# Kernel tuning notes

Measured on AMD Instinct MI355X. Metric: run time of the kernel, lower is better.

Reference implementation:

```python
import jax, jax.numpy as jnp
import numpy as np

N_LBL, E_LBL, K = 32, 16, 16          # node labels, edge labels, tensor_neurons
DN, DE = 2 * N_LBL, 2 * E_LBL         # TNM input dims
REG = [16, 8, 4]                      # reg_neurons
N = M = 6000


def setup_inputs() -> dict:
    key = jax.random.key(0)
    ks = jax.random.split(key, 24)
    u = lambda k, s: jax.random.uniform(k, s, dtype=jnp.float32)
    g = lambda k, s: jax.random.normal(k, s, dtype=jnp.float32) * 0.1
    inp = dict(
        emb1=u(ks[0], (N, N_LBL)), emb2=u(ks[1], (N, N_LBL)),
        adj1=u(ks[2], (N, N)), adj2=u(ks[3], (N, N)),
        edge_attr1=u(ks[4], (M, E_LBL)), edge_attr2=u(ks[5], (M, E_LBL)),
        edge_adj1=u(ks[6], (M, M)), edge_adj2=u(ks[7], (M, M)),
        avg_v=jnp.float32(50.0),
        # tensor networks: nc, in, ie share D=DN (stacked on axis 0); ec uses DE
        Wn=g(ks[8], (3, DN, DN, K)), Wbn=g(ks[9], (3, K, 2 * DN)), bn=g(ks[10], (3, K)),
        We=g(ks[11], (DE, DE, K)), Wbe=g(ks[12], (K, 2 * DE)), be=g(ks[13], (K,)),
        # 4 MLP stacks (order nc, in, ie, ec), torch Linear layout [out, in]
        mlp1_w=g(ks[14], (4, REG[0], K)), mlp1_b=g(ks[15], (4, REG[0])),
        mlp2_w=g(ks[16], (4, REG[1], REG[0])), mlp2_b=g(ks[17], (4, REG[1])),
        mlp3_w=g(ks[18], (4, REG[2], REG[1])), mlp3_b=g(ks[19], (4, REG[2])),
        score_w=g(ks[20], (4, REG[2])), score_b=g(ks[21], (4,)),
    )
    return inp


def _tnm(e1, e2, W, Wb, b):
    # SimGNN-style bilinear tensor network on pooled vectors e1,e2: [D]
    scoring = jnp.einsum('d,dek,e->k', e1, W, e2)
    block = Wb @ jnp.concatenate([e1, e2])
    return jax.nn.relu(scoring + block + b)  # [K]


def reference(emb1, emb2, adj1, adj2, edge_attr1, edge_attr2, edge_adj1, edge_adj2,
              avg_v, Wn, Wbn, bn, We, Wbe, be,
              mlp1_w, mlp1_b, mlp2_w, mlp2_b, mlp3_w, mlp3_b, score_w, score_b):
    def gal_pass(adj, feat):
        h1 = adj @ feat          # GraphAggregationLayer: mm(adj, input)
        h2 = adj @ h1
        return h1, h2

    g1h1, g1h2 = gal_pass(adj1, emb1)
    g2h1, g2h2 = gal_pass(adj2, emb2)
    e1h1, _ = gal_pass(edge_adj1, edge_attr1)
    e2h1, _ = gal_pass(edge_adj2, edge_attr2)

    # concat + sum-pool -> single vectors of width 2D
    g1_01 = jnp.concatenate([emb1, g1h1], axis=1).sum(0)   # [DN]
    g2_01 = jnp.concatenate([emb2, g2h1], axis=1).sum(0)
    g1_12 = jnp.concatenate([g1h1, g1h2], axis=1).sum(0)
    g2_12 = jnp.concatenate([g2h1, g2h2], axis=1).sum(0)
    e1_01 = jnp.concatenate([edge_attr1, e1h1], axis=1).sum(0)  # [DE]
    e2_01 = jnp.concatenate([edge_attr2, e2h1], axis=1).sum(0)

    # node branches nc, in (use 01 pooled) and ie (uses 12 pooled)
    e1s = jnp.stack([g1_01, g1_01, g1_12])
    e2s = jnp.stack([g2_01, g2_01, g2_12])
    s_node = jax.vmap(_tnm)(e1s, e2s, Wn, Wbn, bn)          # [3, K]
    s_ec = _tnm(e1_01, e2_01, We, Wbe, be)                  # [K]
    s = jnp.concatenate([s_node, s_ec[None]], axis=0)       # [4, K] (nc,in,ie,ec)

    h = jax.nn.relu(jnp.einsum('boi,bi->bo', mlp1_w, s) + mlp1_b)
    h = jax.nn.relu(jnp.einsum('boi,bi->bo', mlp2_w, h) + mlp2_b)
    h = jax.nn.relu(jnp.einsum('boi,bi->bo', mlp3_w, h) + mlp3_b)
    scores4 = jax.nn.sigmoid(jnp.einsum('bi,bi->b', score_w, h) + score_b)  # [4]

    # final order: nc, in, ec, ie
    score = scores4[jnp.array([0, 1, 3, 2])]
    pre_ged = jnp.sum(-jnp.log(score) * avg_v)              # target_mode == 'exp'
    pre_sim = jnp.exp(-pre_ged / avg_v)
    return pre_sim, pre_ged, score
```

## Files before the change

### kernel.cpp

```cpp
#include <hip/hip_runtime.h>
#include <cstdint>
#include <cmath>

#define THREADS 256
#define LDP 6016
#define RGROUPS 8
#define SLAB_R 32

template <bool WEIGHTED>
__global__ __launch_bounds__(THREADS, 8)
void colsum_tile_kernel(const float* __restrict__ A0,
                        const float* __restrict__ A1,
                        const float* __restrict__ w0,
                        const float* __restrict__ w1,
                        float* __restrict__ P,
                        int N, int nSlabs, int R) {
    const int z = blockIdx.z;
    const float* __restrict__ A = z ? A1 : A0;
    const float* __restrict__ wv = z ? w1 : w0;

    const int col = blockIdx.x * (THREADS * 4) + threadIdx.x * 4;
    if (col >= N) return;
    const int slab = blockIdx.y;
    int r0 = slab * R;
    int r1 = r0 + R;
    if (r1 > N) r1 = N;

    float ax = 0.f, ay = 0.f, az = 0.f, aw = 0.f;
    float bx = 0.f, by = 0.f, bz = 0.f, bw = 0.f;
    const float* p = A + (size_t)r0 * N + col;
    const size_t sN = (size_t)N;
    int r = r0;
    for (; r + 8 <= r1; r += 8, p += 8 * sN) {
        float4 v0 = *reinterpret_cast<const float4*>(p + 0 * sN);
        float4 v1 = *reinterpret_cast<const float4*>(p + 1 * sN);
        float4 v2 = *reinterpret_cast<const float4*>(p + 2 * sN);
        float4 v3 = *reinterpret_cast<const float4*>(p + 3 * sN);
        float4 v4 = *reinterpret_cast<const float4*>(p + 4 * sN);
        float4 v5 = *reinterpret_cast<const float4*>(p + 5 * sN);
        float4 v6 = *reinterpret_cast<const float4*>(p + 6 * sN);
        float4 v7 = *reinterpret_cast<const float4*>(p + 7 * sN);
        float q0 = WEIGHTED ? wv[r + 0] : 1.f;
        float q1 = WEIGHTED ? wv[r + 1] : 1.f;
        float q2 = WEIGHTED ? wv[r + 2] : 1.f;
        float q3 = WEIGHTED ? wv[r + 3] : 1.f;
        float q4 = WEIGHTED ? wv[r + 4] : 1.f;
        float q5 = WEIGHTED ? wv[r + 5] : 1.f;
        float q6 = WEIGHTED ? wv[r + 6] : 1.f;
        float q7 = WEIGHTED ? wv[r + 7] : 1.f;
        ax += q0 * v0.x; ay += q0 * v0.y; az += q0 * v0.z; aw += q0 * v0.w;
        bx += q1 * v1.x; by += q1 * v1.y; bz += q1 * v1.z; bw += q1 * v1.w;
        ax += q2 * v2.x; ay += q2 * v2.y; az += q2 * v2.z; aw += q2 * v2.w;
        bx += q3 * v3.x; by += q3 * v3.y; bz += q3 * v3.z; bw += q3 * v3.w;
        ax += q4 * v4.x; ay += q4 * v4.y; az += q4 * v4.z; aw += q4 * v4.w;
        bx += q5 * v5.x; by += q5 * v5.y; bz += q5 * v5.z; bw += q5 * v5.w;
        ax += q6 * v6.x; ay += q6 * v6.y; az += q6 * v6.z; aw += q6 * v6.w;
        bx += q7 * v7.x; by += q7 * v7.y; bz += q7 * v7.z; bw += q7 * v7.w;
    }
    for (; r < r1; ++r, p += sN) {
        float4 v = *reinterpret_cast<const float4*>(p);
        float q = WEIGHTED ? wv[r] : 1.f;
        ax += q * v.x; ay += q * v.y; az += q * v.z; aw += q * v.w;
    }
    float4 o = {ax + bx, ay + by, az + bz, aw + bw};
    *reinterpret_cast<float4*>(&P[((size_t)z * nSlabs + slab) * LDP + col]) = o;
}

__global__ void reduce_atomic_kernel(const float* __restrict__ P,
                                     float* __restrict__ out0,
                                     float* __restrict__ out1,
                                     int N, int nSlabs) {
    int col = blockIdx.x * (THREADS * 4) + threadIdx.x * 4;
    if (col >= N) return;
    int z = blockIdx.y;
    int chunk = (nSlabs + RGROUPS - 1) / RGROUPS;
    int i0 = blockIdx.z * chunk;
    int i1 = i0 + chunk;
    if (i1 > nSlabs) i1 = nSlabs;
    float* out = z ? out1 : out0;

    const float* p = P + ((size_t)z * nSlabs + i0) * LDP + col;
    float4 s0 = {0, 0, 0, 0}, s1 = {0, 0, 0, 0};
    int i = i0;
    for (; i + 2 <= i1; i += 2, p += 2 * LDP) {
        float4 a = *reinterpret_cast<const float4*>(p);
        float4 b = *reinterpret_cast<const float4*>(p + LDP);
        s0.x += a.x; s0.y += a.y; s0.z += a.z; s0.w += a.w;
        s1.x += b.x; s1.y += b.y; s1.z += b.z; s1.w += b.w;
    }
    if (i < i1) {
        float4 a = *reinterpret_cast<const float4*>(p);
        s0.x += a.x; s0.y += a.y; s0.z += a.z; s0.w += a.w;
    }
    atomicAdd(&out[col + 0], s0.x + s1.x);
    atomicAdd(&out[col + 1], s0.y + s1.y);
    atomicAdd(&out[col + 2], s0.z + s1.z);
    atomicAdd(&out[col + 3], s0.w + s1.w);
}

__global__ void feat_all_kernel(const float* __restrict__ emb1,
                                const float* __restrict__ emb2,
                                const float* __restrict__ eat1,
                                const float* __restrict__ eat2,
                                const float* __restrict__ c1,
                                const float* __restrict__ d1,
                                const float* __restrict__ c2,
                                const float* __restrict__ d2,
                                const float* __restrict__ ce1,
                                const float* __restrict__ ce2,
                                float* __restrict__ n1,
                                float* __restrict__ n2,
                                float* __restrict__ eg1,
                                float* __restrict__ eg2,
                                int Nn, int Ne) {
    int unit = blockIdx.y;
    const float *feat, *c, *d;
    float* out;
    int total, log2L;
    bool hasQ;
    if (unit == 0)      { feat = emb1; c = c1;  d = d1;      out = n1;  total = Nn * 32; log2L = 5; hasQ = true;  }
    else if (unit == 1) { feat = emb2; c = c2;  d = d2;      out = n2;  total = Nn * 32; log2L = 5; hasQ = true;  }
    else if (unit == 2) { feat = eat1; c = ce1; d = nullptr; out = eg1; total = Ne * 16; log2L = 4; hasQ = false; }
    else                { feat = eat2; c = ce2; d = nullptr; out = eg2; total = Ne * 16; log2L = 4; hasQ = false; }

    int stride = gridDim.x * blockDim.x;
    int idx = blockIdx.x * blockDim.x + threadIdx.x;
    int L = 1 << log2L;
    int l = idx & (L - 1);
    float as = 0.f, ap = 0.f, aq = 0.f;
    for (int i = idx; i < total; i += stride) {
        float v = feat[i];
        int r = i >> log2L;
        as += v;
        ap += c[r] * v;
        if (hasQ) aq += d[r] * v;
    }
    atomicAdd(&out[l], as);
    atomicAdd(&out[L + l], ap);
    if (hasQ) atomicAdd(&out[2 * L + l], aq);
}

__global__ void scoring_kernel(const float* __restrict__ Wn,
                               const float* __restrict__ We,
                               const float* __restrict__ n1,
                               const float* __restrict__ n2,
                               const float* __restrict__ eg1,
                               const float* __restrict__ eg2,
                               float* __restrict__ scoring) {
    int b = blockIdx.y;
    int chunk = blockIdx.x;
    const float *W, *e1, *e2;
    int total, log2D;
    if (b < 3) {
        W = Wn + (size_t)b * (64 * 64 * 16);
        e1 = n1 + (b == 2 ? 32 : 0);
        e2 = n2 + (b == 2 ? 32 : 0);
        total = 64 * 64 * 16;
        log2D = 6;
    } else {
        W = We;
        e1 = eg1;
        e2 = eg2;
        total = 32 * 32 * 16;
        log2D = 5;
    }
    int begin = chunk * 4096 + threadIdx.x;
    int end = (chunk + 1) * 4096;
    if (end > total) end = total;
    float acc = 0.f;
    for (int idx = begin; idx < end; idx += 256) {
        int de = idx >> 4;
        int e = de & ((1 << log2D) - 1);
        int dd = de >> log2D;
        acc += e1[dd] * e2[e] * W[idx];
    }
    __shared__ float red[256];
    red[threadIdx.x] = acc;
    __syncthreads();
    if (threadIdx.x < 16) {
        float s = 0.f;
        for (int t = threadIdx.x; t < 256; t += 16) s += red[t];
        atomicAdd(&scoring[b * 16 + threadIdx.x], s);
    }
}

__global__ void final_kernel(const float* __restrict__ scoring,
                             const float* __restrict__ n1,
                             const float* __restrict__ n2,
                             const float* __restrict__ eg1,
                             const float* __restrict__ eg2,
                             const float* __restrict__ Wbn,
                             const float* __restrict__ bn,
                             const float* __restrict__ Wbe,
                             const float* __restrict__ be,
                             const float* __restrict__ m1w,
                             const float* __restrict__ m1b,
                             const float* __restrict__ m2w,
                             const float* __restrict__ m2b,
                             const float* __restrict__ m3w,
                             const float* __restrict__ m3b,
                             const float* __restrict__ sw,
                             const float* __restrict__ sb,
                             const float* __restrict__ avg_v,
                             float* __restrict__ out) {
    __shared__ float sval[4][16];
    __shared__ float scores[4];
    int t = threadIdx.x;
    int b = t >> 4, k = t & 15;

    float blk;
    if (b < 3) {
        const float* e1 = n1 + (b == 2 ? 32 : 0);
        const float* e2 = n2 + (b == 2 ? 32 : 0);
        const float* wb = Wbn + (size_t)b * (16 * 128) + k * 128;
        float s = 0.f;
        for (int j = 0; j < 64; ++j) s += wb[j] * e1[j];
        for (int j = 0; j < 64; ++j) s += wb[64 + j] * e2[j];
        blk = s + bn[b * 16 + k];
    } else {
        const float* wb = Wbe + k * 64;
        float s = 0.f;
        for (int j = 0; j < 32; ++j) s += wb[j] * eg1[j];
        for (int j = 0; j < 32; ++j) s += wb[32 + j] * eg2[j];
        blk = s + be[k];
    }
    float v = scoring[b * 16 + k] + blk;
    sval[b][k] = v > 0.f ? v : 0.f;
    __syncthreads();

    if (t < 4) {
        float h1[16], h2[8], h3[4];
        for (int o = 0; o < 16; ++o) {
            float a = m1b[t * 16 + o];
            for (int i = 0; i < 16; ++i) a += m1w[(t * 16 + o) * 16 + i] * sval[t][i];
            h1[o] = a > 0.f ? a : 0.f;
        }
        for (int o = 0; o < 8; ++o) {
            float a = m2b[t * 8 + o];
            for (int i = 0; i < 16; ++i) a += m2w[(t * 8 + o) * 16 + i] * h1[i];
            h2[o] = a > 0.f ? a : 0.f;
        }
        for (int o = 0; o < 4; ++o) {
            float a = m3b[t * 4 + o];
            for (int i = 0; i < 8; ++i) a += m3w[(t * 4 + o) * 8 + i] * h2[i];
            h3[o] = a > 0.f ? a : 0.f;
        }
        float z = sb[t];
        for (int i = 0; i < 4; ++i) z += sw[t * 4 + i] * h3[i];
        scores[t] = 1.0f / (1.0f + expf(-z));
    }
    __syncthreads();

    if (t == 0) {
        const int ord[4] = {0, 1, 3, 2};
        float av = avg_v[0];
        float acc = 0.f;
        for (int j = 0; j < 4; ++j) {
            float sc = scores[ord[j]];
            out[2 + j] = sc;
            acc += -logf(sc);
        }
        float ged = acc * av;
        out[1] = ged;
        out[0] = expf(-ged / av);
    }
}

extern "C" void kernel_launch(void* const* d_in, const int* in_sizes, int n_in,
                              void* d_out, int out_size, void* d_ws, size_t ws_size,
                              hipStream_t stream) {
    const float* emb1  = (const float*)d_in[0];
    const float* emb2  = (const float*)d_in[1];
    const float* adj1  = (const float*)d_in[2];
    const float* adj2  = (const float*)d_in[3];
    const float* eat1  = (const float*)d_in[4];
    const float* eat2  = (const float*)d_in[5];
    const float* eadj1 = (const float*)d_in[6];
    const float* eadj2 = (const float*)d_in[7];
    const float* avg_v = (const float*)d_in[8];
    const float* Wn    = (const float*)d_in[9];
    const float* Wbn   = (const float*)d_in[10];
    const float* bn    = (const float*)d_in[11];
    const float* We    = (const float*)d_in[12];
    const float* Wbe   = (const float*)d_in[13];
    const float* be    = (const float*)d_in[14];
    const float* m1w   = (const float*)d_in[15];
    const float* m1b   = (const float*)d_in[16];
    const float* m2w   = (const float*)d_in[17];
    const float* m2b   = (const float*)d_in[18];
    const float* m3w   = (const float*)d_in[19];
    const float* m3b   = (const float*)d_in[20];
    const float* sw    = (const float*)d_in[21];
    const float* sb    = (const float*)d_in[22];

    int Nn = in_sizes[0] / 32;
    int Ne = in_sizes[4] / 16;
    int N = Nn;

    size_t availF = ws_size / 4;
    size_t reserveF = 8 * (size_t)N + 4096;
    size_t perMat = (availF > reserveF) ? (availF - reserveF) / 2 : 0;
    int maxSlabs = (int)(perMat / LDP);
    int nSlabs = (N + SLAB_R - 1) / SLAB_R;
    if (nSlabs > maxSlabs) nSlabs = maxSlabs > 0 ? maxSlabs : 1;
    int R = (N + nSlabs - 1) / nSlabs;
    nSlabs = (N + R - 1) / R;

    float* ws  = (float*)d_ws;
    float* P   = ws;
    float* c1  = P + (size_t)2 * nSlabs * LDP;
    float* d1  = c1 + N;
    float* c2  = d1 + N;
    float* d2  = c2 + N;
    float* ce1 = d2 + N;
    float* ce2 = ce1 + N;
    float* n1  = ce2 + N;
    float* n2  = n1 + 96;
    float* eg1 = n2 + 96;
    float* eg2 = eg1 + 32;
    float* scoring = eg2 + 32;
    hipMemsetAsync(c1, 0, (6 * (size_t)N + 320) * sizeof(float), stream);

    dim3 blk(THREADS);
    int colChunks = (N + THREADS * 4 - 1) / (THREADS * 4);
    dim3 gridS(colChunks, nSlabs, 2);
    dim3 gridR(colChunks, 2, RGROUPS);

    colsum_tile_kernel<false><<<gridS, blk, 0, stream>>>(adj1, adj2, nullptr, nullptr, P, N, nSlabs, R);
    reduce_atomic_kernel<<<gridR, blk, 0, stream>>>(P, c1, c2, N, nSlabs);
    colsum_tile_kernel<true ><<<gridS, blk, 0, stream>>>(adj1, adj2, c1, c2, P, N, nSlabs, R);
    reduce_atomic_kernel<<<gridR, blk, 0, stream>>>(P, d1, d2, N, nSlabs);
    colsum_tile_kernel<false><<<gridS, blk, 0, stream>>>(eadj1, eadj2, nullptr, nullptr, P, N, nSlabs, R);
    reduce_atomic_kernel<<<gridR, blk, 0, stream>>>(P, ce1, ce2, N, nSlabs);

    feat_all_kernel<<<dim3(16, 4), blk, 0, stream>>>(emb1, emb2, eat1, eat2,
                                                     c1, d1, c2, d2, ce1, ce2,
                                                     n1, n2, eg1, eg2, Nn, Ne);

    scoring_kernel<<<dim3(16, 4), blk, 0, stream>>>(Wn, We, n1, n2, eg1, eg2, scoring);

    final_kernel<<<1, 64, 0, stream>>>(scoring, n1, n2, eg1, eg2,
                                       Wbn, bn, Wbe, be,
                                       m1w, m1b, m2w, m2b, m3w, m3b, sw, sb,
                                       avg_v, (float*)d_out);
}
```

Before: 236.8 us.

## Fuse node adjacency colsum with A@emb tile product to read adjacency once

Replaces the two column-sum passes over each node adjacency (plain, then weighted by the first colsum) with one tiled kernel. That kernel loads each adjacency tile into shared memory, emits the partial column sums, and also accumulates per-row partial products A@emb into a chunked buffer. The second-hop pooled term is then recovered in the feature kernel as the colsum-weighted sum of those row products. This cuts one full pass of HBM traffic over both 6000x6000 matrices, at the cost of an LDS-bound FMA inner loop, unpipelined tile loads with block-wide syncs, and extra workspace for the chunked partial products.

```diff
diff --git a/kernel.cpp b/kernel.cpp
--- a/kernel.cpp
+++ b/kernel.cpp
@@ -5,20 +5,137 @@
 #define THREADS 256
 #define LDP 6016
 #define RGROUPS 8
-#define SLAB_R 32
-
-template <bool WEIGHTED>
+#define EDGE_R 64
+#define TI 64
+#define TJ 128
+#define ASTR 129
+#define ESTR 36
+
+__global__ __launch_bounds__(THREADS)
+void node_pass_kernel(const float* __restrict__ A0, const float* __restrict__ A1,
+                      const float* __restrict__ E0, const float* __restrict__ E1,
+                      float* __restrict__ Pc,
+                      float* __restrict__ PH,
+                      int N, int strips, int chunkW, int nch) {
+    const int z = blockIdx.z;
+    const float* __restrict__ A = z ? A1 : A0;
+    const float* __restrict__ E = z ? E1 : E0;
+    const int strip = blockIdx.y;
+    const int r0 = strip * TI;
+    const int rows = min(TI, N - r0);
+    const int chunk = blockIdx.x;
+    const int j0c = chunk * chunkW;
+    const int j1c = min(j0c + chunkW, N);
+
+    __shared__ float At[TI * ASTR];
+    __shared__ float Et[TJ * ESTR];
+
+    const int t = threadIdx.x;
+    const int rg = t & 15;
+    const int lg = (t >> 4) & 3;
+    const int jg = t >> 6;
+
+    float acc[4][8];
+#pragma unroll
+    for (int k = 0; k < 4; ++k)
+#pragma unroll
+        for (int u = 0; u < 8; ++u) acc[k][u] = 0.f;
+
+    for (int jt = j0c; jt < j1c; jt += TJ) {
+        __syncthreads();
+#pragma unroll
+        for (int p = 0; p < 8; ++p) {
+            int f = t + p * THREADS;
+            int r = f >> 5;
+            int c4 = f & 31;
+            int gj = jt + (c4 << 2);
+            float4 v = {0.f, 0.f, 0.f, 0.f};
+            if (r < rows && gj < j1c)
+                v = *reinterpret_cast<const float4*>(&A[(size_t)(r0 + r) * N + gj]);
+            float* dst = &At[r * ASTR + (c4 << 2)];
+            dst[0] = v.x; dst[1] = v.y; dst[2] = v.z; dst[3] = v.w;
+        }
+#pragma unroll
+        for (int p = 0; p < 4; ++p) {
+            int f = t + p * THREADS;
+            int jr = f >> 3;
+            int l4 = (f & 7) << 2;
+            int gj = jt + jr;
+            float4 v = {0.f, 0.f, 0.f, 0.f};
+            if (gj < j1c)
+                v = *reinterpret_cast<const float4*>(&E[(size_t)gj * 32 + l4]);
+            *reinterpret_cast<float4*>(&Et[jr * ESTR + l4]) = v;
+        }
+        __syncthreads();
+        const int jb = jg * 32;
+#pragma unroll 4
+        for (int jj = 0; jj < 32; ++jj) {
+            const int j = jb + jj;
+            const float a0 = At[(4 * rg + 0) * ASTR + j];
+            const float a1 = At[(4 * rg + 1) * ASTR + j];
+            const float a2 = At[(4 * rg + 2) * ASTR + j];
+            const float a3 = At[(4 * rg + 3) * ASTR + j];
+            const float4 eA = *reinterpret_cast<const float4*>(&Et[j * ESTR + 8 * lg]);
+            const float4 eB = *reinterpret_cast<const float4*>(&Et[j * ESTR + 8 * lg + 4]);
+            const float e[8] = {eA.x, eA.y, eA.z, eA.w, eB.x, eB.y, eB.z, eB.w};
+#pragma unroll
+            for (int u = 0; u < 8; ++u) {
+                acc[0][u] += a0 * e[u];
+                acc[1][u] += a1 * e[u];
+                acc[2][u] += a2 * e[u];
+                acc[3][u] += a3 * e[u];
+            }
+        }
+        if (t < TJ) {
+            int gj = jt + t;
+            if (gj < j1c) {
+                float s = 0.f;
+#pragma unroll
+                for (int r = 0; r < TI; ++r) s += At[r * ASTR + t];
+                Pc[((size_t)z * strips + strip) * LDP + gj] = s;
+            }
+        }
+    }
+
+    __syncthreads();
+    float* buf = At;
+    for (int s = 0; s < 4; ++s) {
+        if (jg == s) {
+#pragma unroll
+            for (int k = 0; k < 4; ++k) {
+                float* b = &buf[(4 * rg + k) * 33 + 8 * lg];
+                if (s == 0) {
+#pragma unroll
+                    for (int u = 0; u < 8; ++u) b[u] = acc[k][u];
+                } else {
+#pragma unroll
+                    for (int u = 0; u < 8; ++u) b[u] += acc[k][u];
+                }
+            }
+        }
+        __syncthreads();
+    }
+    {
+        int rr = t >> 2;
+        int l8 = (t & 3) * 8;
+        if (rr < rows) {
+            const float* b = &buf[rr * 33 + l8];
+            float4 v0 = {b[0], b[1], b[2], b[3]};
+            float4 v1 = {b[4], b[5], b[6], b[7]};
+            size_t off = (((size_t)z * nch + chunk) * N + (r0 + rr)) * 32 + l8;
+            *reinterpret_cast<float4*>(&PH[off]) = v0;
+            *reinterpret_cast<float4*>(&PH[off + 4]) = v1;
+        }
+    }
+}
+
 __global__ __launch_bounds__(THREADS, 8)
 void colsum_tile_kernel(const float* __restrict__ A0,
                         const float* __restrict__ A1,
-                        const float* __restrict__ w0,
-                        const float* __restrict__ w1,
                         float* __restrict__ P,
                         int N, int nSlabs, int R) {
     const int z = blockIdx.z;
     const float* __restrict__ A = z ? A1 : A0;
-    const float* __restrict__ wv = z ? w1 : w0;
-
     const int col = blockIdx.x * (THREADS * 4) + threadIdx.x * 4;
     if (col >= N) return;
     const int slab = blockIdx.y;
@@ -40,27 +157,18 @@
         float4 v5 = *reinterpret_cast<const float4*>(p + 5 * sN);
         float4 v6 = *reinterpret_cast<const float4*>(p + 6 * sN);
         float4 v7 = *reinterpret_cast<const float4*>(p + 7 * sN);
-        float q0 = WEIGHTED ? wv[r + 0] : 1.f;
-        float q1 = WEIGHTED ? wv[r + 1] : 1.f;
-        float q2 = WEIGHTED ? wv[r + 2] : 1.f;
-        float q3 = WEIGHTED ? wv[r + 3] : 1.f;
-        float q4 = WEIGHTED ? wv[r + 4] : 1.f;
-        float q5 = WEIGHTED ? wv[r + 5] : 1.f;
-        float q6 = WEIGHTED ? wv[r + 6] : 1.f;
-        float q7 = WEIGHTED ? wv[r + 7] : 1.f;
-        ax += q0 * v0.x; ay += q0 * v0.y; az += q0 * v0.z; aw += q0 * v0.w;
-        bx += q1 * v1.x; by += q1 * v1.y; bz += q1 * v1.z; bw += q1 * v1.w;
-        ax += q2 * v2.x; ay += q2 * v2.y; az += q2 * v2.z; aw += q2 * v2.w;
-        bx += q3 * v3.x; by += q3 * v3.y; bz += q3 * v3.z; bw += q3 * v3.w;
-        ax += q4 * v4.x; ay += q4 * v4.y; az += q4 * v4.z; aw += q4 * v4.w;
-        bx += q5 * v5.x; by += q5 * v5.y; bz += q5 * v5.z; bw += q5 * v5.w;
-        ax += q6 * v6.x; ay += q6 * v6.y; az += q6 * v6.z; aw += q6 * v6.w;
-        bx += q7 * v7.x; by += q7 * v7.y; bz += q7 * v7.z; bw += q7 * v7.w;
+        ax += v0.x; ay += v0.y; az += v0.z; aw += v0.w;
+        bx += v1.x; by += v1.y; bz += v1.z; bw += v1.w;
+        ax += v2.x; ay += v2.y; az += v2.z; aw += v2.w;
+        bx += v3.x; by += v3.y; bz += v3.z; bw += v3.w;
+        ax += v4.x; ay += v4.y; az += v4.z; aw += v4.w;
+        bx += v5.x; by += v5.y; bz += v5.z; bw += v5.w;
+        ax += v6.x; ay += v6.y; az += v6.z; aw += v6.w;
+        bx += v7.x; by += v7.y; bz += v7.z; bw += v7.w;
     }
     for (; r < r1; ++r, p += sN) {
         float4 v = *reinterpret_cast<const float4*>(p);
-        float q = WEIGHTED ? wv[r] : 1.f;
-        ax += q * v.x; ay += q * v.y; az += q * v.z; aw += q * v.w;
+        ax += v.x; ay += v.y; az += v.z; aw += v.w;
     }
     float4 o = {ax + bx, ay + by, az + bz, aw + bw};
     *reinterpret_cast<float4*>(&P[((size_t)z * nSlabs + slab) * LDP + col]) = o;
@@ -98,46 +206,45 @@
     atomicAdd(&out[col + 3], s0.w + s1.w);
 }
 
-__global__ void feat_all_kernel(const float* __restrict__ emb1,
-                                const float* __restrict__ emb2,
-                                const float* __restrict__ eat1,
-                                const float* __restrict__ eat2,
-                                const float* __restrict__ c1,
-                                const float* __restrict__ d1,
-                                const float* __restrict__ c2,
-                                const float* __restrict__ d2,
-                                const float* __restrict__ ce1,
-                                const float* __restrict__ ce2,
-                                float* __restrict__ n1,
-                                float* __restrict__ n2,
-                                float* __restrict__ eg1,
-                                float* __restrict__ eg2,
-                                int Nn, int Ne) {
+__global__ void feat_all_kernel(const float* __restrict__ emb1, const float* __restrict__ emb2,
+                                const float* __restrict__ eat1, const float* __restrict__ eat2,
+                                const float* __restrict__ PH,
+                                const float* __restrict__ c1, const float* __restrict__ c2,
+                                const float* __restrict__ ce1, const float* __restrict__ ce2,
+                                float* __restrict__ n1, float* __restrict__ n2,
+                                float* __restrict__ eg1, float* __restrict__ eg2,
+                                int Nn, int Ne, int nch) {
     int unit = blockIdx.y;
-    const float *feat, *c, *d;
-    float* out;
+    const float* feat = nullptr; const float* w = nullptr; const float* ph = nullptr;
+    float* outS = nullptr; float* outP = nullptr;
     int total, log2L;
-    bool hasQ;
-    if (unit == 0)      { feat = emb1; c = c1;  d = d1;      out = n1;  total = Nn * 32; log2L = 5; hasQ = true;  }
-    else if (unit == 1) { feat = emb2; c = c2;  d = d2;      out = n2;  total = Nn * 32; log2L = 5; hasQ = true;  }
-    else if (unit == 2) { feat = eat1; c = ce1; d = nullptr; out = eg1; total = Ne * 16; log2L = 4; hasQ = false; }
-    else                { feat = eat2; c = ce2; d = nullptr; out = eg2; total = Ne * 16; log2L = 4; hasQ = false; }
+    if (unit == 0)      { feat = emb1; w = c1;  outS = n1;  outP = n1 + 32;  total = Nn * 32; log2L = 5; }
+    else if (unit == 1) { feat = emb2; w = c2;  outS = n2;  outP = n2 + 32;  total = Nn * 32; log2L = 5; }
+    else if (unit == 2) { feat = eat1; w = ce1; outS = eg1; outP = eg1 + 16; total = Ne * 16; log2L = 4; }
+    else if (unit == 3) { feat = eat2; w = ce2; outS = eg2; outP = eg2 + 16; total = Ne * 16; log2L = 4; }
+    else if (unit == 4) { ph = PH;                              w = c1; outP = n1 + 64; total = Nn * 32; log2L = 5; }
+    else                { ph = PH + (size_t)nch * Nn * 32;      w = c2; outP = n2 + 64; total = Nn * 32; log2L = 5; }
 
     int stride = gridDim.x * blockDim.x;
     int idx = blockIdx.x * blockDim.x + threadIdx.x;
     int L = 1 << log2L;
     int l = idx & (L - 1);
-    float as = 0.f, ap = 0.f, aq = 0.f;
-    for (int i = idx; i < total; i += stride) {
-        float v = feat[i];
-        int r = i >> log2L;
-        as += v;
-        ap += c[r] * v;
-        if (hasQ) aq += d[r] * v;
-    }
-    atomicAdd(&out[l], as);
-    atomicAdd(&out[L + l], ap);
-    if (hasQ) atomicAdd(&out[2 * L + l], aq);
+    float as = 0.f, ap = 0.f;
+    if (ph) {
+        for (int i = idx; i < total; i += stride) {
+            float v = 0.f;
+            for (int ch = 0; ch < nch; ++ch) v += ph[(size_t)ch * total + i];
+            ap += w[i >> log2L] * v;
+        }
+    } else {
+        for (int i = idx; i < total; i += stride) {
+            float v = feat[i];
+            as += v;
+            ap += w[i >> log2L] * v;
+        }
+        atomicAdd(&outS[l], as);
+    }
+    atomicAdd(&outP[l], ap);
 }
 
 __global__ void scoring_kernel(const float* __restrict__ Wn,
@@ -158,9 +265,7 @@
         total = 64 * 64 * 16;
         log2D = 6;
     } else {
-        W = We;
-        e1 = eg1;
-        e2 = eg2;
+        W = We; e1 = eg1; e2 = eg2;
         total = 32 * 32 * 16;
         log2D = 5;
     }
@@ -193,14 +298,10 @@
                              const float* __restrict__ bn,
                              const float* __restrict__ Wbe,
                              const float* __restrict__ be,
-                             const float* __restrict__ m1w,
-                             const float* __restrict__ m1b,
-                             const float* __restrict__ m2w,
-                             const float* __restrict__ m2b,
-                             const float* __restrict__ m3w,
-                             const float* __restrict__ m3b,
-                             const float* __restrict__ sw,
-                             const float* __restrict__ sb,
+                             const float* __restrict__ m1w, const float* __restrict__ m1b,
+                             const float* __restrict__ m2w, const float* __restrict__ m2b,
+                             const float* __restrict__ m3w, const float* __restrict__ m3b,
+                             const float* __restrict__ sw, const float* __restrict__ sb,
                              const float* __restrict__ avg_v,
                              float* __restrict__ out) {
     __shared__ float sval[4][16];
@@ -295,50 +396,46 @@
 
     int Nn = in_sizes[0] / 32;
     int Ne = in_sizes[4] / 16;
-    int N = Nn;
-
-    size_t availF = ws_size / 4;
-    size_t reserveF = 8 * (size_t)N + 4096;
-    size_t perMat = (availF > reserveF) ? (availF - reserveF) / 2 : 0;
-    int maxSlabs = (int)(perMat / LDP);
-    int nSlabs = (N + SLAB_R - 1) / SLAB_R;
-    if (nSlabs > maxSlabs) nSlabs = maxSlabs > 0 ? maxSlabs : 1;
-    int R = (N + nSlabs - 1) / nSlabs;
-    nSlabs = (N + R - 1) / R;
+    int N  = Nn;
+
+    int strips = (N + TI - 1) / TI;
+    int eSlabs = (N + EDGE_R - 1) / EDGE_R;
+
+    size_t pFloats = (size_t)2 * strips * LDP;
+    int nch = 4;
+    while (nch > 1) {
+        size_t need = (pFloats + (size_t)2 * nch * N * 32 + 4 * (size_t)N + 512) * 4;
+        if (need <= ws_size) break;
+        nch >>= 1;
+    }
+    int chunkW = (((N + nch - 1) / nch) + 3) & ~3;
 
     float* ws  = (float*)d_ws;
     float* P   = ws;
-    float* c1  = P + (size_t)2 * nSlabs * LDP;
-    float* d1  = c1 + N;
-    float* c2  = d1 + N;
-    float* d2  = c2 + N;
-    float* ce1 = d2 + N;
+    float* PH  = P + pFloats;
+    float* c1  = PH + (size_t)2 * nch * N * 32;
+    float* c2  = c1 + N;
+    float* ce1 = c2 + N;
     float* ce2 = ce1 + N;
     float* n1  = ce2 + N;
     float* n2  = n1 + 96;
     float* eg1 = n2 + 96;
     float* eg2 = eg1 + 32;
     float* scoring = eg2 + 32;
-    hipMemsetAsync(c1, 0, (6 * (size_t)N + 320) * sizeof(float), stream);
+    hipMemsetAsync(c1, 0, (4 * (size_t)N + 320) * sizeof(float), stream);
 
     dim3 blk(THREADS);
     int colChunks = (N + THREADS * 4 - 1) / (THREADS * 4);
-    dim3 gridS(colChunks, nSlabs, 2);
-    dim3 gridR(colChunks, 2, RGROUPS);
-
-    colsum_tile_kernel<false><<<gridS, blk, 0, stream>>>(adj1, adj2, nullptr, nullptr, P, N, nSlabs, R);
-    reduce_atomic_kernel<<<gridR, blk, 0, stream>>>(P, c1, c2, N, nSlabs);
-    colsum_tile_kernel<true ><<<gridS, blk, 0, stream>>>(adj1, adj2, c1, c2, P, N, nSlabs, R);
-    reduce_atomic_kernel<<<gridR, blk, 0, stream>>>(P, d1, d2, N, nSlabs);
-    colsum_tile_kernel<false><<<gridS, blk, 0, stream>>>(eadj1, eadj2, nullptr, nullptr, P, N, nSlabs, R);
-    reduce_atomic_kernel<<<gridR, blk, 0, stream>>>(P, ce1, ce2, N, nSlabs);
-
-    feat_all_kernel<<<dim3(16, 4), blk, 0, stream>>>(emb1, emb2, eat1, eat2,
-                                                     c1, d1, c2, d2, ce1, ce2,
-                                                     n1, n2, eg1, eg2, Nn, Ne);
-
+
+    node_pass_kernel<<<dim3(nch, strips, 2), blk, 0, stream>>>(
+        adj1, adj2, emb1, emb2, P, PH, N, strips, chunkW, nch);
+    reduce_atomic_kernel<<<dim3(colChunks, 2, RGROUPS), blk, 0, stream>>>(P, c1, c2, N, strips);
+    colsum_tile_kernel<<<dim3(colChunks, eSlabs, 2), blk, 0, stream>>>(eadj1, eadj2, P, N, eSlabs, EDGE_R);
+    reduce_atomic_kernel<<<dim3(colChunks, 2, RGROUPS), blk, 0, stream>>>(P, ce1, ce2, N, eSlabs);
+    feat_all_kernel<<<dim3(16, 6), blk, 0, stream>>>(emb1, emb2, eat1, eat2, PH,
+                                                     c1, c2, ce1, ce2,
+                                                     n1, n2, eg1, eg2, Nn, Ne, nch);
     scoring_kernel<<<dim3(16, 4), blk, 0, stream>>>(Wn, We, n1, n2, eg1, eg2, scoring);
-
     final_kernel<<<1, 64, 0, stream>>>(scoring, n1, n2, eg1, eg2,
                                        Wbn, bn, Wbe, be,
                                        m1w, m1b, m2w, m2b, m3w, m3b, sw, sb,
```

Result: slower. 322.7 us (+36.3%).

## Batch unweighted column sums into one launch, reorder to keep adjacency hot in cache

Applied to the files above, without the earlier changes.

The two unweighted column-sum passes (edge adjacency and node adjacency) now run in a single four-matrix launch, with a matching four-output reduction, cutting launches. Edge matrices use nontemporal loads. Node adjacency is read last with normal loads so it may stay in the large last-level cache for the following weighted pass. Slab height doubles to 64 rows and the workspace-size clamp is removed, so a small workspace could now overflow.

```diff
diff --git a/kernel.cpp b/kernel.cpp
--- a/kernel.cpp
+++ b/kernel.cpp
@@ -5,20 +5,16 @@
 #define THREADS 256
 #define LDP 6016
 #define RGROUPS 8
-#define SLAB_R 32
-
-template <bool WEIGHTED>
+#define SLAB_R 64
+
+typedef float vf4 __attribute__((ext_vector_type(4)));
+
 __global__ __launch_bounds__(THREADS, 8)
-void colsum_tile_kernel(const float* __restrict__ A0,
-                        const float* __restrict__ A1,
-                        const float* __restrict__ w0,
-                        const float* __restrict__ w1,
-                        float* __restrict__ P,
-                        int N, int nSlabs, int R) {
+void colsum4_kernel(const float* __restrict__ M0, const float* __restrict__ M1,
+                    const float* __restrict__ M2, const float* __restrict__ M3,
+                    float* __restrict__ P, int N, int nSlabs, int R) {
     const int z = blockIdx.z;
-    const float* __restrict__ A = z ? A1 : A0;
-    const float* __restrict__ wv = z ? w1 : w0;
-
+    const float* __restrict__ A = (z == 0) ? M0 : (z == 1) ? M1 : (z == 2) ? M2 : M3;
     const int col = blockIdx.x * (THREADS * 4) + threadIdx.x * 4;
     if (col >= N) return;
     const int slab = blockIdx.y;
@@ -31,23 +27,83 @@
     const float* p = A + (size_t)r0 * N + col;
     const size_t sN = (size_t)N;
     int r = r0;
+    if (z < 2) {
+        for (; r + 8 <= r1; r += 8, p += 8 * sN) {
+            vf4 v0 = __builtin_nontemporal_load((const vf4*)(p + 0 * sN));
+            vf4 v1 = __builtin_nontemporal_load((const vf4*)(p + 1 * sN));
+            vf4 v2 = __builtin_nontemporal_load((const vf4*)(p + 2 * sN));
+            vf4 v3 = __builtin_nontemporal_load((const vf4*)(p + 3 * sN));
+            vf4 v4 = __builtin_nontemporal_load((const vf4*)(p + 4 * sN));
+            vf4 v5 = __builtin_nontemporal_load((const vf4*)(p + 5 * sN));
+            vf4 v6 = __builtin_nontemporal_load((const vf4*)(p + 6 * sN));
+            vf4 v7 = __builtin_nontemporal_load((const vf4*)(p + 7 * sN));
+            ax += v0.x; ay += v0.y; az += v0.z; aw += v0.w;
+            bx += v1.x; by += v1.y; bz += v1.z; bw += v1.w;
+            ax += v2.x; ay += v2.y; az += v2.z; aw += v2.w;
+            bx += v3.x; by += v3.y; bz += v3.z; bw += v3.w;
+            ax += v4.x; ay += v4.y; az += v4.z; aw += v4.w;
+            bx += v5.x; by += v5.y; bz += v5.z; bw += v5.w;
+            ax += v6.x; ay += v6.y; az += v6.z; aw += v6.w;
+            bx += v7.x; by += v7.y; bz += v7.z; bw += v7.w;
+        }
+    } else {
+        for (; r + 8 <= r1; r += 8, p += 8 * sN) {
+            vf4 v0 = *(const vf4*)(p + 0 * sN);
+            vf4 v1 = *(const vf4*)(p + 1 * sN);
+            vf4 v2 = *(const vf4*)(p + 2 * sN);
+            vf4 v3 = *(const vf4*)(p + 3 * sN);
+            vf4 v4 = *(const vf4*)(p + 4 * sN);
+            vf4 v5 = *(const vf4*)(p + 5 * sN);
+            vf4 v6 = *(const vf4*)(p + 6 * sN);
+            vf4 v7 = *(const vf4*)(p + 7 * sN);
+            ax += v0.x; ay += v0.y; az += v0.z; aw += v0.w;
+            bx += v1.x; by += v1.y; bz += v1.z; bw += v1.w;
+            ax += v2.x; ay += v2.y; az += v2.z; aw += v2.w;
+            bx += v3.x; by += v3.y; bz += v3.z; bw += v3.w;
+            ax += v4.x; ay += v4.y; az += v4.z; aw += v4.w;
+            bx += v5.x; by += v5.y; bz += v5.z; bw += v5.w;
+            ax += v6.x; ay += v6.y; az += v6.z; aw += v6.w;
+            bx += v7.x; by += v7.y; bz += v7.z; bw += v7.w;
+        }
+    }
+    for (; r < r1; ++r, p += sN) {
+        vf4 v = *(const vf4*)(p);
+        ax += v.x; ay += v.y; az += v.z; aw += v.w;
+    }
+    float4 o = {ax + bx, ay + by, az + bz, aw + bw};
+    *reinterpret_cast<float4*>(&P[((size_t)z * nSlabs + slab) * LDP + col]) = o;
+}
+
+__global__ __launch_bounds__(THREADS, 8)
+void colsum2w_kernel(const float* __restrict__ A0, const float* __restrict__ A1,
+                     const float* __restrict__ w0, const float* __restrict__ w1,
+                     float* __restrict__ P, int N, int nSlabs, int R) {
+    const int z = blockIdx.z;
+    const float* __restrict__ A = z ? A1 : A0;
+    const float* __restrict__ wv = z ? w1 : w0;
+    const int col = blockIdx.x * (THREADS * 4) + threadIdx.x * 4;
+    if (col >= N) return;
+    const int slab = blockIdx.y;
+    int r0 = slab * R;
+    int r1 = r0 + R;
+    if (r1 > N) r1 = N;
+
+    float ax = 0.f, ay = 0.f, az = 0.f, aw = 0.f;
+    float bx = 0.f, by = 0.f, bz = 0.f, bw = 0.f;
+    const float* p = A + (size_t)r0 * N + col;
+    const size_t sN = (size_t)N;
+    int r = r0;
     for (; r + 8 <= r1; r += 8, p += 8 * sN) {
-        float4 v0 = *reinterpret_cast<const float4*>(p + 0 * sN);
-        float4 v1 = *reinterpret_cast<const float4*>(p + 1 * sN);
-        float4 v2 = *reinterpret_cast<const float4*>(p + 2 * sN);
-        float4 v3 = *reinterpret_cast<const float4*>(p + 3 * sN);
-        float4 v4 = *reinterpret_cast<const float4*>(p + 4 * sN);
-        float4 v5 = *reinterpret_cast<const float4*>(p + 5 * sN);
-        float4 v6 = *reinterpret_cast<const float4*>(p + 6 * sN);
-        float4 v7 = *reinterpret_cast<const float4*>(p + 7 * sN);
-        float q0 = WEIGHTED ? wv[r + 0] : 1.f;
-        float q1 = WEIGHTED ? wv[r + 1] : 1.f;
-        float q2 = WEIGHTED ? wv[r + 2] : 1.f;
-        float q3 = WEIGHTED ? wv[r + 3] : 1.f;
-        float q4 = WEIGHTED ? wv[r + 4] : 1.f;
-        float q5 = WEIGHTED ? wv[r + 5] : 1.f;
-        float q6 = WEIGHTED ? wv[r + 6] : 1.f;
-        float q7 = WEIGHTED ? wv[r + 7] : 1.f;
+        vf4 v0 = *(const vf4*)(p + 0 * sN);
+        vf4 v1 = *(const vf4*)(p + 1 * sN);
+        vf4 v2 = *(const vf4*)(p + 2 * sN);
+        vf4 v3 = *(const vf4*)(p + 3 * sN);
+        vf4 v4 = *(const vf4*)(p + 4 * sN);
+        vf4 v5 = *(const vf4*)(p + 5 * sN);
+        vf4 v6 = *(const vf4*)(p + 6 * sN);
+        vf4 v7 = *(const vf4*)(p + 7 * sN);
+        float q0 = wv[r + 0], q1 = wv[r + 1], q2 = wv[r + 2], q3 = wv[r + 3];
+        float q4 = wv[r + 4], q5 = wv[r + 5], q6 = wv[r + 6], q7 = wv[r + 7];
         ax += q0 * v0.x; ay += q0 * v0.y; az += q0 * v0.z; aw += q0 * v0.w;
         bx += q1 * v1.x; by += q1 * v1.y; bz += q1 * v1.z; bw += q1 * v1.w;
         ax += q2 * v2.x; ay += q2 * v2.y; az += q2 * v2.z; aw += q2 * v2.w;
@@ -58,26 +114,26 @@
         bx += q7 * v7.x; by += q7 * v7.y; bz += q7 * v7.z; bw += q7 * v7.w;
     }
     for (; r < r1; ++r, p += sN) {
-        float4 v = *reinterpret_cast<const float4*>(p);
-        float q = WEIGHTED ? wv[r] : 1.f;
+        vf4 v = *(const vf4*)(p);
+        float q = wv[r];
         ax += q * v.x; ay += q * v.y; az += q * v.z; aw += q * v.w;
     }
     float4 o = {ax + bx, ay + by, az + bz, aw + bw};
     *reinterpret_cast<float4*>(&P[((size_t)z * nSlabs + slab) * LDP + col]) = o;
 }
 
-__global__ void reduce_atomic_kernel(const float* __restrict__ P,
-                                     float* __restrict__ out0,
-                                     float* __restrict__ out1,
-                                     int N, int nSlabs) {
+__global__ void reduce4_kernel(const float* __restrict__ P,
+                               float* __restrict__ o0, float* __restrict__ o1,
+                               float* __restrict__ o2, float* __restrict__ o3,
+                               int N, int nSlabs) {
     int col = blockIdx.x * (THREADS * 4) + threadIdx.x * 4;
     if (col >= N) return;
     int z = blockIdx.y;
+    float* out = (z == 0) ? o0 : (z == 1) ? o1 : (z == 2) ? o2 : o3;
     int chunk = (nSlabs + RGROUPS - 1) / RGROUPS;
     int i0 = blockIdx.z * chunk;
     int i1 = i0 + chunk;
     if (i1 > nSlabs) i1 = nSlabs;
-    float* out = z ? out1 : out0;
 
     const float* p = P + ((size_t)z * nSlabs + i0) * LDP + col;
     float4 s0 = {0, 0, 0, 0}, s1 = {0, 0, 0, 0};
@@ -98,20 +154,13 @@
     atomicAdd(&out[col + 3], s0.w + s1.w);
 }
 
-__global__ void feat_all_kernel(const float* __restrict__ emb1,
-                                const float* __restrict__ emb2,
-                                const float* __restrict__ eat1,
-                                const float* __restrict__ eat2,
-                                const float* __restrict__ c1,
-                                const float* __restrict__ d1,
-                                const float* __restrict__ c2,
-                                const float* __restrict__ d2,
-                                const float* __restrict__ ce1,
-                                const float* __restrict__ ce2,
-                                float* __restrict__ n1,
-                                float* __restrict__ n2,
-                                float* __restrict__ eg1,
-                                float* __restrict__ eg2,
+__global__ void feat_all_kernel(const float* __restrict__ emb1, const float* __restrict__ emb2,
+                                const float* __restrict__ eat1, const float* __restrict__ eat2,
+                                const float* __restrict__ c1, const float* __restrict__ d1,
+                                const float* __restrict__ c2, const float* __restrict__ d2,
+                                const float* __restrict__ ce1, const float* __restrict__ ce2,
+                                float* __restrict__ n1, float* __restrict__ n2,
+                                float* __restrict__ eg1, float* __restrict__ eg2,
                                 int Nn, int Ne) {
     int unit = blockIdx.y;
     const float *feat, *c, *d;
@@ -158,9 +207,7 @@
         total = 64 * 64 * 16;
         log2D = 6;
     } else {
-        W = We;
-        e1 = eg1;
-        e2 = eg2;
+        W = We; e1 = eg1; e2 = eg2;
         total = 32 * 32 * 16;
         log2D = 5;
     }
@@ -193,14 +240,10 @@
                              const float* __restrict__ bn,
                              const float* __restrict__ Wbe,
                              const float* __restrict__ be,
-                             const float* __restrict__ m1w,
-                             const float* __restrict__ m1b,
-                             const float* __restrict__ m2w,
-                             const float* __restrict__ m2b,
-                             const float* __restrict__ m3w,
-                             const float* __restrict__ m3b,
-                             const float* __restrict__ sw,
-                             const float* __restrict__ sb,
+                             const float* __restrict__ m1w, const float* __restrict__ m1b,
+                             const float* __restrict__ m2w, const float* __restrict__ m2b,
+                             const float* __restrict__ m3w, const float* __restrict__ m3b,
+                             const float* __restrict__ sw, const float* __restrict__ sb,
                              const float* __restrict__ avg_v,
                              float* __restrict__ out) {
     __shared__ float sval[4][16];
@@ -295,26 +338,19 @@
 
     int Nn = in_sizes[0] / 32;
     int Ne = in_sizes[4] / 16;
-    int N = Nn;
-
-    size_t availF = ws_size / 4;
-    size_t reserveF = 8 * (size_t)N + 4096;
-    size_t perMat = (availF > reserveF) ? (availF - reserveF) / 2 : 0;
-    int maxSlabs = (int)(perMat / LDP);
+    int N  = Nn;
+
     int nSlabs = (N + SLAB_R - 1) / SLAB_R;
-    if (nSlabs > maxSlabs) nSlabs = maxSlabs > 0 ? maxSlabs : 1;
-    int R = (N + nSlabs - 1) / nSlabs;
-    nSlabs = (N + R - 1) / R;
 
     float* ws  = (float*)d_ws;
     float* P   = ws;
-    float* c1  = P + (size_t)2 * nSlabs * LDP;
-    float* d1  = c1 + N;
-    float* c2  = d1 + N;
-    float* d2  = c2 + N;
-    float* ce1 = d2 + N;
+    float* c1  = P + (size_t)4 * nSlabs * LDP;
+    float* c2  = c1 + N;
+    float* ce1 = c2 + N;
     float* ce2 = ce1 + N;
-    float* n1  = ce2 + N;
+    float* d1  = ce2 + N;
+    float* d2  = d1 + N;
+    float* n1  = d2 + N;
     float* n2  = n1 + 96;
     float* eg1 = n2 + 96;
     float* eg2 = eg1 + 32;
@@ -323,22 +359,19 @@
 
     dim3 blk(THREADS);
     int colChunks = (N + THREADS * 4 - 1) / (THREADS * 4);
-    dim3 gridS(colChunks, nSlabs, 2);
-    dim3 gridR(colChunks, 2, RGROUPS);
-
-    colsum_tile_kernel<false><<<gridS, blk, 0, stream>>>(adj1, adj2, nullptr, nullptr, P, N, nSlabs, R);
-    reduce_atomic_kernel<<<gridR, blk, 0, stream>>>(P, c1, c2, N, nSlabs);
-    colsum_tile_kernel<true ><<<gridS, blk, 0, stream>>>(adj1, adj2, c1, c2, P, N, nSlabs, R);
-    reduce_atomic_kernel<<<gridR, blk, 0, stream>>>(P, d1, d2, N, nSlabs);
-    colsum_tile_kernel<false><<<gridS, blk, 0, stream>>>(eadj1, eadj2, nullptr, nullptr, P, N, nSlabs, R);
-    reduce_atomic_kernel<<<gridR, blk, 0, stream>>>(P, ce1, ce2, N, nSlabs);
-
+
+    colsum4_kernel<<<dim3(colChunks, nSlabs, 4), blk, 0, stream>>>(
+        eadj1, eadj2, adj1, adj2, P, N, nSlabs, SLAB_R);
+    reduce4_kernel<<<dim3(colChunks, 4, RGROUPS), blk, 0, stream>>>(
+        P, ce1, ce2, c1, c2, N, nSlabs);
+    colsum2w_kernel<<<dim3(colChunks, nSlabs, 2), blk, 0, stream>>>(
+        adj1, adj2, c1, c2, P, N, nSlabs, SLAB_R);
+    reduce4_kernel<<<dim3(colChunks, 2, RGROUPS), blk, 0, stream>>>(
+        P, d1, d2, d1, d2, N, nSlabs);
     feat_all_kernel<<<dim3(16, 4), blk, 0, stream>>>(emb1, emb2, eat1, eat2,
                                                      c1, d1, c2, d2, ce1, ce2,
                                                      n1, n2, eg1, eg2, Nn, Ne);
-
     scoring_kernel<<<dim3(16, 4), blk, 0, stream>>>(Wn, We, n1, n2, eg1, eg2, scoring);
-
     final_kernel<<<1, 64, 0, stream>>>(scoring, n1, n2, eg1, eg2,
                                        Wbn, bn, Wbe, be,
                                        m1w, m1b, m2w, m2b, m3w, m3b, sw, sb,
```

Result: faster. 208.1 us, median of 2 (-12.1%).
